# Kernel tuning notes

Hardware: AMD Instinct MI355X
Metric: run time of the kernel (lower is better)

## Reference

```python
import jax, jax.numpy as jnp
import numpy as np

N, E = 50000, 800000
NODE_DIM, EDGE_DIM = 128, 32
EGO_H, PEER_H, EDGE_H = 64, 64, 32  # node_hidden=128 split; edge_hidden=32


def setup_inputs() -> dict:
    key = jax.random.key(0)
    ks = jax.random.split(key, 9)
    x = jax.random.normal(ks[0], (N, NODE_DIM), dtype=jnp.float32)
    edge_attrs = jax.random.normal(ks[1], (E, EDGE_DIM), dtype=jnp.float32)
    edge_index = jax.random.randint(ks[2], (2, E), 0, N, dtype=jnp.int32)
    # Linear params (torch convention: W [out, in]), num_layers=1 -> single emb Linear per MLPLayer
    def lin(k, out_d, in_d):
        kw, kb = jax.random.split(k)
        s = 1.0 / np.sqrt(in_d)
        return (jax.random.uniform(kw, (out_d, in_d), minval=-s, maxval=s, dtype=jnp.float32),
                jax.random.uniform(kb, (out_d,), minval=-s, maxval=s, dtype=jnp.float32))
    W_peer, b_peer = lin(ks[3], PEER_H + EDGE_H, NODE_DIM + EDGE_DIM)
    W_ego, b_ego = lin(ks[4], EGO_H, NODE_DIM)
    W_edge, b_edge = lin(ks[5], EDGE_H, EDGE_DIM)
    return {"x": x, "edge_attrs": edge_attrs,
            "W_peer": W_peer, "b_peer": b_peer,
            "W_ego": W_ego, "b_ego": b_ego,
            "W_edge": W_edge, "b_edge": b_edge,
            "edge_index": edge_index}


def reference(x, edge_attrs, W_peer, b_peer, W_ego, b_ego, W_edge, b_edge, edge_index):
    n = x.shape[0]
    # adj_t = SparseTensor(row=ei[0], col=ei[1]).t() -> row = ei[1], col = ei[0]
    row = edge_index[1]
    col = edge_index[0]

    # ego branch
    h_ego = jax.nn.relu(x @ W_ego.T + b_ego)  # [N, EGO_H]

    # degree-based row normalization: deg^-0.5 per adj_t row, inf -> 0
    deg = jax.ops.segment_sum(jnp.ones((row.shape[0],), x.dtype), row, num_segments=n)
    dinv = jnp.where(deg > 0, jax.lax.rsqrt(jnp.maximum(deg, 1.0)) * (deg > 0), 0.0)
    dinv = jnp.where(deg > 0, deg ** -0.5, 0.0)
    norm_val = dinv[row]  # [E]

    # peer branch: gather x[row], cat edge_attrs, linear, normalize, scatter-sum over row
    peer_features = jnp.concatenate([x[row], edge_attrs], axis=1)  # [E, NODE_DIM+EDGE_DIM]
    peer_msg = norm_val[:, None] * (peer_features @ W_peer.T + b_peer)
    h_peer = jax.nn.relu(jax.ops.segment_sum(peer_msg, row, num_segments=n))  # [N, PEER_H+EDGE_H]

    # edge branch
    h_e = jax.nn.relu(edge_attrs @ W_edge.T + b_edge)  # [E, EDGE_H]
    h_e_agg = jax.ops.segment_sum(h_e, row, num_segments=n)  # adj_t.set_value(h_edge).sum(1)
    # norm.matmul(h_edge): out[i] = sum_{e: row[e]==i} norm_val[e] * h_e_agg[col[e]]
    h_e_mm = jax.ops.segment_sum(norm_val[:, None] * h_e_agg[col], row, num_segments=n)
    h_edge = jnp.concatenate([h_e_agg, h_e_mm], axis=1)  # [N, 2*EDGE_H]

    out = jnp.concatenate([h_ego, h_edge, h_peer], axis=1)  # [N, 224]
    return out
```

## Files before the change

kernel.cpp:

```cpp
#include <hip/hip_runtime.h>


typedef float f32x4 __attribute__((ext_vector_type(4)));
typedef short bf16x8 __attribute__((ext_vector_type(8)));
typedef unsigned short u16x8 __attribute__((ext_vector_type(8)));

#define BP 256

__device__ __forceinline__ unsigned short f2bf(float f) {
    unsigned u = __float_as_uint(f);
    u += 0x7fffu + ((u >> 16) & 1u);
    return (unsigned short)(u >> 16);
}
__device__ __forceinline__ float bf2f(unsigned short u) {
    return __uint_as_float((unsigned)u << 16);
}
__device__ __forceinline__ u16x8 pk8u(float4 lo, float4 hi) {
    u16x8 r;
    r[0]=f2bf(lo.x); r[1]=f2bf(lo.y); r[2]=f2bf(lo.z); r[3]=f2bf(lo.w);
    r[4]=f2bf(hi.x); r[5]=f2bf(hi.y); r[6]=f2bf(hi.z); r[7]=f2bf(hi.w);
    return r;
}
__device__ __forceinline__ bf16x8 mk_frag(ushort4 lo, ushort4 hi) {
    bf16x8 b;
    b[0]=(short)lo.x; b[1]=(short)lo.y; b[2]=(short)lo.z; b[3]=(short)lo.w;
    b[4]=(short)hi.x; b[5]=(short)hi.y; b[6]=(short)hi.z; b[7]=(short)hi.w;
    return b;
}
__device__ __forceinline__ bf16x8 ld_bfrag(const unsigned short* bp) {
    return mk_frag(*reinterpret_cast<const ushort4*>(bp),
                   *reinterpret_cast<const ushort4*>(bp + 16));
}

__global__ __launch_bounds__(256) void k_prepw(const float* __restrict__ W_ego,
                                               const float* __restrict__ W_peer,
                                               const float* __restrict__ W_edge,
                                               unsigned short* __restrict__ Bt,
                                               unsigned short* __restrict__ Bte,
                                               int* __restrict__ deg, int N) {
    int idx = blockIdx.x * blockDim.x + threadIdx.x;
    if (idx < 160 * 160) {
        int n = idx / 160, k = idx % 160;
        float v;
        if (n < 64) v = (k < 128) ? W_ego[n * 128 + k] : 0.f;
        else        v = W_peer[(n - 64) * 160 + k];
        Bt[idx] = f2bf(v);
    } else if (idx < 160 * 160 + 32 * 32) {
        int j = idx - 160 * 160;
        Bte[j] = f2bf(W_edge[j]);
    }
    if (idx < N) deg[idx] = 0;
}

__global__ __launch_bounds__(256) void k_hist(const int* __restrict__ row,
                                              int* __restrict__ deg,
                                              int* __restrict__ rank, int E) {
    int e = blockIdx.x * blockDim.x + threadIdx.x;
    if (e < E) rank[e] = atomicAdd(&deg[row[e]], 1);
}

__global__ __launch_bounds__(256) void k_scan_partial(const int* __restrict__ deg,
                                                      int* __restrict__ bsum, int N) {
    __shared__ int sh[256];
    int base = blockIdx.x * 1024 + threadIdx.x * 4;
    int s = 0;
#pragma unroll
    for (int q = 0; q < 4; ++q) { int i = base + q; if (i < N) s += deg[i]; }
    sh[threadIdx.x] = s;
    __syncthreads();
    for (int off = 128; off > 0; off >>= 1) {
        if (threadIdx.x < off) sh[threadIdx.x] += sh[threadIdx.x + off];
        __syncthreads();
    }
    if (threadIdx.x == 0) bsum[blockIdx.x] = sh[0];
}

__global__ __launch_bounds__(256) void k_scan_final(
    const int* __restrict__ deg, const int* __restrict__ bsum,
    int* __restrict__ off,
    float* __restrict__ sd, float* __restrict__ rdeg, int* __restrict__ nstart,
    float* __restrict__ eagg, float* __restrict__ sea, int N)
{
    __shared__ int sh[256];
    __shared__ int s_boff;
    int t = threadIdx.x;
    int NB = gridDim.x;

    if (t < 64) {
        int v = (t < NB) ? bsum[t] : 0;
        int p = (t < (int)blockIdx.x) ? v : 0;
#pragma unroll
        for (int m = 1; m < 64; m <<= 1) {
            p += __shfl_xor(p, m);
            v += __shfl_xor(v, m);
        }
        if (t == 0) {
            s_boff = p;
            if (blockIdx.x == 0) off[N] = v;
        }
    }
    __syncthreads();

    int base = blockIdx.x * 1024 + t * 4;
    int v[4];
#pragma unroll
    for (int q = 0; q < 4; ++q) v[q] = (base + q < N) ? deg[base + q] : 0;
    int ts = v[0] + v[1] + v[2] + v[3];
    sh[t] = ts;
    __syncthreads();
    int incl = ts;
    for (int d = 1; d < 256; d <<= 1) {
        int val = (t >= d) ? sh[t - d] : 0;
        __syncthreads();
        incl += val;
        sh[t] = incl;
        __syncthreads();
    }
    int running = s_boff + incl - ts;
#pragma unroll
    for (int q = 0; q < 4; ++q) {
        int i = base + q;
        if (i < N) {
            int s = running, e = running + v[q];
            off[i] = s;
            int dg = v[q];
            sd[i]   = dg > 0 ? sqrtf((float)dg) : 0.f;
            rdeg[i] = dg > 0 ? 1.f / (float)dg : 0.f;
            for (int b = (s + BP - 1) / BP; b * BP < e; ++b) nstart[b] = i;
            bool zneed = (dg == 0) || ((s / BP) != ((e - 1) / BP));
            if (zneed) {
                float4 z = {0.f, 0.f, 0.f, 0.f};
                float4* pe = reinterpret_cast<float4*>(eagg + (size_t)i * 32);
                float4* ps = reinterpret_cast<float4*>(sea  + (size_t)i * 32);
#pragma unroll
                for (int q2 = 0; q2 < 8; ++q2) { pe[q2] = z; ps[q2] = z; }
            }
            running = e;
        }
    }
}

__global__ __launch_bounds__(256) void k_scatcvt(
    const float* __restrict__ ea, const int* __restrict__ row,
    const int* __restrict__ col, const int* __restrict__ off,
    const int* __restrict__ rank,
    unsigned short* __restrict__ easorted,
    unsigned short* __restrict__ colsort, int E)
{
    int e = blockIdx.x * blockDim.x + threadIdx.x;
    if (e >= E) return;
    int pos = off[row[e]] + rank[e];
    const float4* src = reinterpret_cast<const float4*>(ea + (size_t)e * 32);
    u16x8* dst = reinterpret_cast<u16x8*>(easorted + (size_t)pos * 32);
#pragma unroll
    for (int q = 0; q < 4; ++q)
        dst[q] = pk8u(src[2 * q], src[2 * q + 1]);
    colsort[pos] = (unsigned short)col[e];
}

__global__ __launch_bounds__(512) void k_agg(
    const unsigned short* __restrict__ easorted,
    const int* __restrict__ off, const int* __restrict__ nstart,
    const unsigned short* __restrict__ Bte, const float* __restrict__ b_edge,
    float* __restrict__ eagg, float* __restrict__ sea, int N, int E)
{
    __shared__ unsigned short hs [BP][36];
    __shared__ unsigned short asr[BP][36];
    const int tid  = threadIdx.x;
    const int w    = tid >> 6;
    const int lane = tid & 63;
    const int n16  = lane & 15;
    const int h    = lane >> 4;
    const int P    = blockIdx.x * BP;

    {
        const int tA = w * 32 + n16;
        const int p0 = min(P + tA,      E - 1);
        const int p1 = min(P + tA + 16, E - 1);
        const unsigned short* r0 = easorted + (size_t)p0 * 32 + h * 4;
        const unsigned short* r1 = easorted + (size_t)p1 * 32 + h * 4;
        ushort4 lo0 = *reinterpret_cast<const ushort4*>(r0);
        ushort4 hi0 = *reinterpret_cast<const ushort4*>(r0 + 16);
        ushort4 lo1 = *reinterpret_cast<const ushort4*>(r1);
        ushort4 hi1 = *reinterpret_cast<const ushort4*>(r1 + 16);

        *reinterpret_cast<ushort4*>(&asr[tA][h * 4])           = lo0;
        *reinterpret_cast<ushort4*>(&asr[tA][16 + h * 4])      = hi0;
        *reinterpret_cast<ushort4*>(&asr[tA + 16][h * 4])      = lo1;
        *reinterpret_cast<ushort4*>(&asr[tA + 16][16 + h * 4]) = hi1;

        bf16x8 a0 = mk_frag(lo0, hi0);
        bf16x8 a1 = mk_frag(lo1, hi1);
        bf16x8 b0 = ld_bfrag(Bte + (size_t)n16 * 32 + h * 4);
        bf16x8 b1 = ld_bfrag(Bte + (size_t)(16 + n16) * 32 + h * 4);
        f32x4 d00 = {0.f,0.f,0.f,0.f}, d01 = {0.f,0.f,0.f,0.f};
        f32x4 d10 = {0.f,0.f,0.f,0.f}, d11 = {0.f,0.f,0.f,0.f};
        d00 = __builtin_amdgcn_mfma_f32_16x16x32_bf16(a0, b0, d00, 0, 0, 0);
        d01 = __builtin_amdgcn_mfma_f32_16x16x32_bf16(a0, b1, d01, 0, 0, 0);
        d10 = __builtin_amdgcn_mfma_f32_16x16x32_bf16(a1, b0, d10, 0, 0, 0);
        d11 = __builtin_amdgcn_mfma_f32_16x16x32_bf16(a1, b1, d11, 0, 0, 0);

        const int tr0 = w * 32 + h * 4;
        float be0 = b_edge[n16], be1 = b_edge[16 + n16];
#pragma unroll
        for (int r = 0; r < 4; ++r) {
            hs[tr0 + r][n16]           = f2bf(fmaxf(d00[r] + be0, 0.f));
            hs[tr0 + r][16 + n16]      = f2bf(fmaxf(d01[r] + be1, 0.f));
            hs[tr0 + 16 + r][n16]      = f2bf(fmaxf(d10[r] + be0, 0.f));
            hs[tr0 + 16 + r][16 + n16] = f2bf(fmaxf(d11[r] + be1, 0.f));
        }
    }
    __syncthreads();

    const int c = lane & 7, sub = lane >> 3;
    const int node0 = nstart[blockIdx.x];

    for (int n = node0 + w; n < N; n += 8) {
        int s0 = off[n];
        if (s0 >= P + BP) break;
        int e0 = off[n + 1];
        int s = max(s0, P) - P, eEnd = min(e0, P + BP) - P;
        float4 hv = {0.f,0.f,0.f,0.f}, av = {0.f,0.f,0.f,0.f};
        for (int t = s + sub; t < eEnd; t += 8) {
            ushort4 uh = *reinterpret_cast<const ushort4*>(&hs [t][c * 4]);
            ushort4 ua = *reinterpret_cast<const ushort4*>(&asr[t][c * 4]);
            hv.x += bf2f(uh.x); hv.y += bf2f(uh.y); hv.z += bf2f(uh.z); hv.w += bf2f(uh.w);
            av.x += bf2f(ua.x); av.y += bf2f(ua.y); av.z += bf2f(ua.z); av.w += bf2f(ua.w);
        }
#pragma unroll
        for (int m = 8; m < 64; m <<= 1) {
            hv.x += __shfl_xor(hv.x, m); hv.y += __shfl_xor(hv.y, m);
            hv.z += __shfl_xor(hv.z, m); hv.w += __shfl_xor(hv.w, m);
            av.x += __shfl_xor(av.x, m); av.y += __shfl_xor(av.y, m);
            av.z += __shfl_xor(av.z, m); av.w += __shfl_xor(av.w, m);
        }
        if (lane < 8) {
            float* pe = eagg + (size_t)n * 32 + c * 4;
            float* ps = sea  + (size_t)n * 32 + c * 4;
            bool interior = (s0 >= P) && (e0 <= P + BP);
            if (interior) {
                *reinterpret_cast<float4*>(pe) = hv;
                *reinterpret_cast<float4*>(ps) = av;
            } else {
                atomicAdd(pe+0,hv.x); atomicAdd(pe+1,hv.y);
                atomicAdd(pe+2,hv.z); atomicAdd(pe+3,hv.w);
                atomicAdd(ps+0,av.x); atomicAdd(ps+1,av.y);
                atomicAdd(ps+2,av.z); atomicAdd(ps+3,av.w);
            }
        }
    }
}

__global__ __launch_bounds__(256) void k_nodecvt(
    const float* __restrict__ x, const float* __restrict__ sea,
    const float* __restrict__ sd, const float* __restrict__ rdeg,
    const unsigned short* __restrict__ Bt,
    const float* __restrict__ b_ego, const float* __restrict__ b_peer,
    const float* __restrict__ eagg, unsigned short* __restrict__ eagg_bf,
    float* __restrict__ out, int N, int node_grid)
{
    if ((int)blockIdx.x >= node_grid) {
        int idx = (blockIdx.x - node_grid) * 256 + threadIdx.x;
        if (idx >= N * 8) return;
        int node = idx >> 3, c = idx & 7;
        float4 v = reinterpret_cast<const float4*>(eagg + (size_t)node * 32)[c];
        ushort4 u = {f2bf(v.x), f2bf(v.y), f2bf(v.z), f2bf(v.w)};
        *reinterpret_cast<ushort4*>(eagg_bf + (size_t)node * 32 + c * 4) = u;
        reinterpret_cast<float4*>(out + (size_t)node * 224 + 64)[c] = v;
        return;
    }
    const int lane = threadIdx.x & 63;
    const int wv   = threadIdx.x >> 6;
    const int wm   = blockIdx.x * 64 + wv * 16;
    const int n16  = lane & 15;
    const int h    = lane >> 4;

    const int m_l = min(wm + n16, N - 1);

    f32x4 acc[10];
#pragma unroll
    for (int f = 0; f < 10; ++f) acc[f] = (f32x4){0.f,0.f,0.f,0.f};

#pragma unroll
    for (int kc = 0; kc < 5; ++kc) {
        bf16x8 bfr[10];
#pragma unroll
        for (int f = 0; f < 10; ++f)
            bfr[f] = ld_bfrag(Bt + (size_t)(f * 16 + n16) * 160 + kc * 32 + h * 4);
        float4 lo, hi;
        if (kc < 4) {
            const float* ap = x + (size_t)m_l * 128 + kc * 32 + h * 4;
            lo = *reinterpret_cast<const float4*>(ap);
            hi = *reinterpret_cast<const float4*>(ap + 16);
        } else {
            float r = rdeg[m_l];
            const float* ap = sea + (size_t)m_l * 32 + h * 4;
            lo = *reinterpret_cast<const float4*>(ap);
            hi = *reinterpret_cast<const float4*>(ap + 16);
            lo.x*=r; lo.y*=r; lo.z*=r; lo.w*=r;
            hi.x*=r; hi.y*=r; hi.z*=r; hi.w*=r;
        }
        u16x8 au = pk8u(lo, hi);
        bf16x8 a;
#pragma unroll
        for (int q = 0; q < 8; ++q) a[q] = (short)au[q];
#pragma unroll
        for (int f = 0; f < 10; ++f)
            acc[f] = __builtin_amdgcn_mfma_f32_16x16x32_bf16(a, bfr[f], acc[f], 0, 0, 0);
    }

    const int r4 = h * 4;
    float sdv[4];
#pragma unroll
    for (int r = 0; r < 4; ++r) {
        int node = wm + r4 + r;
        sdv[r] = (node < N) ? sd[node] : 0.f;
    }
#pragma unroll
    for (int f = 0; f < 10; ++f) {
        int c = f * 16 + n16;
        float be = (c < 64)  ? b_ego[c] : 0.f;
        float bp = (c >= 64) ? b_peer[c - 64] : 0.f;
#pragma unroll
        for (int r = 0; r < 4; ++r) {
            int node = wm + r4 + r;
            if (node >= N) continue;
            float v = acc[f][r];
            if (c < 64)
                out[(size_t)node * 224 + c] = fmaxf(v + be, 0.f);
            else
                out[(size_t)node * 224 + 64 + c] = fmaxf(sdv[r] * (v + bp), 0.f);
        }
    }
}

__global__ __launch_bounds__(256) void k_mmagg(
    const unsigned short* __restrict__ colsort, const int* __restrict__ off,
    const unsigned short* __restrict__ eagg_bf, float* __restrict__ out, int N)
{
    int wid  = (blockIdx.x * blockDim.x + threadIdx.x) >> 6;
    int lane = threadIdx.x & 63;
    if (wid >= N) return;
    int s = off[wid], e = off[wid + 1];
    int c   = lane & 7;
    int sub = lane >> 3;
    float4 acc = {0.f, 0.f, 0.f, 0.f};
    float4 acc2 = {0.f, 0.f, 0.f, 0.f};
    for (int t0 = s; t0 < e; t0 += 16) {
        int t1 = t0 + sub, t2 = t0 + 8 + sub;
        if (t1 < e) {
            ushort4 u = *reinterpret_cast<const ushort4*>(
                eagg_bf + (size_t)colsort[t1] * 32 + c * 4);
            acc.x += bf2f(u.x); acc.y += bf2f(u.y);
            acc.z += bf2f(u.z); acc.w += bf2f(u.w);
        }
        if (t2 < e) {
            ushort4 u = *reinterpret_cast<const ushort4*>(
                eagg_bf + (size_t)colsort[t2] * 32 + c * 4);
            acc2.x += bf2f(u.x); acc2.y += bf2f(u.y);
            acc2.z += bf2f(u.z); acc2.w += bf2f(u.w);
        }
    }
    acc.x += acc2.x; acc.y += acc2.y; acc.z += acc2.z; acc.w += acc2.w;
#pragma unroll
    for (int m = 8; m < 64; m <<= 1) {
        acc.x += __shfl_xor(acc.x, m);
        acc.y += __shfl_xor(acc.y, m);
        acc.z += __shfl_xor(acc.z, m);
        acc.w += __shfl_xor(acc.w, m);
    }
    int dg = e - s;
    float dinv = dg > 0 ? rsqrtf((float)dg) : 0.f;
    if (lane < 8) {
        float4 o4 = {acc.x * dinv, acc.y * dinv, acc.z * dinv, acc.w * dinv};
        reinterpret_cast<float4*>(out + (size_t)wid * 224 + 96)[c] = o4;
    }
}

extern "C" void kernel_launch(void* const* d_in, const int* in_sizes, int n_in,
                              void* d_out, int out_size, void* d_ws, size_t ws_size,
                              hipStream_t stream)
{
    const float* x      = (const float*)d_in[0];
    const float* ea     = (const float*)d_in[1];
    const float* W_peer = (const float*)d_in[2];
    const float* b_peer = (const float*)d_in[3];
    const float* W_ego  = (const float*)d_in[4];
    const float* b_ego  = (const float*)d_in[5];
    const float* W_edge = (const float*)d_in[6];
    const float* b_edge = (const float*)d_in[7];
    const int*   ei     = (const int*)d_in[8];

    const int N = in_sizes[0] / 128;
    const int E = in_sizes[8] / 2;
    const int* col = ei;
    const int* row = ei + E;
    const int nblocks = (E + BP - 1) / BP;

    char* wp = (char*)d_ws;
    auto carve = [&](size_t bytes) { char* r = wp; wp += (bytes + 15) & ~(size_t)15; return r; };
    int*            rank     = (int*)carve((size_t)E * 4);
    unsigned short* easorted = (unsigned short*)carve((size_t)E * 64);
    unsigned short* colsort  = (unsigned short*)carve((size_t)E * 2);
    int*            deg_i    = (int*)carve((size_t)N * 4);
    float*          eagg     = (float*)carve((size_t)N * 128);
    float*          sea      = (float*)carve((size_t)N * 128);
    unsigned short* eagg_bf  = (unsigned short*)carve((size_t)N * 64);
    int*            off      = (int*)carve((size_t)(N + 1) * 4);
    int*            bsum     = (int*)carve(64 * 4);
    float*          sd       = (float*)carve((size_t)N * 4);
    float*          rdeg     = (float*)carve((size_t)N * 4);
    int*            nstart   = (int*)carve((size_t)nblocks * 4);
    unsigned short* Bt       = (unsigned short*)carve(160 * 160 * 2);
    unsigned short* Bte      = (unsigned short*)carve(32 * 32 * 2);
    float*          out      = (float*)d_out;

    const int TB = 256;
    const int NB = (N + 1023) / 1024;
    const int prepn = max(N, 160 * 160 + 32 * 32);
    k_prepw       <<<(prepn + TB - 1) / TB, TB, 0, stream>>>(W_ego, W_peer, W_edge,
                                                             Bt, Bte, deg_i, N);
    k_hist        <<<(E + TB - 1) / TB, TB, 0, stream>>>(row, deg_i, rank, E);
    k_scan_partial<<<NB, TB, 0, stream>>>(deg_i, bsum, N);
    k_scan_final  <<<NB, TB, 0, stream>>>(deg_i, bsum, off, sd, rdeg,
                                          nstart, eagg, sea, N);
    k_scatcvt     <<<(E + TB - 1) / TB, TB, 0, stream>>>(ea, row, col, off, rank,
                                                         easorted, colsort, E);

    k_agg<<<nblocks, 512, 0, stream>>>(easorted, off, nstart, Bte, b_edge,
                                       eagg, sea, N, E);

    const int node_grid = (N + 63) / 64;
    const int cvt_grid  = (N * 8 + TB - 1) / TB;
    k_nodecvt<<<node_grid + cvt_grid, TB, 0, stream>>>(x, sea, sd, rdeg, Bt,
                                                       b_ego, b_peer, eagg,
                                                       eagg_bf, out, N, node_grid);

    const int agg_grid = (N + 3) / 4;
    k_mmagg<<<agg_grid, TB, 0, stream>>>(colsort, off, eagg_bf, out, N);
}
```

Before: 190.5 us.

## Fuse edge-aggregate output and bf16 conversion into k_agg; vectorize scatter

k_agg now writes interior-node edge aggregates directly to the output and to the bf16 copy. The later conversion pass only handles nodes that span block boundaries or have zero degree, which it detects from offsets. k_scatcvt processes four edges per thread with vectorized int4 loads of row, rank and col. This is meant to cut redundant global reads and writes of the edge aggregate and reduce the launch and thread overhead of the scatter.

```diff
diff --git a/kernel.cpp b/kernel.cpp
--- a/kernel.cpp
+++ b/kernel.cpp
@@ -147,22 +147,46 @@
     unsigned short* __restrict__ easorted,
     unsigned short* __restrict__ colsort, int E)
 {
-    int e = blockIdx.x * blockDim.x + threadIdx.x;
-    if (e >= E) return;
-    int pos = off[row[e]] + rank[e];
-    const float4* src = reinterpret_cast<const float4*>(ea + (size_t)e * 32);
-    u16x8* dst = reinterpret_cast<u16x8*>(easorted + (size_t)pos * 32);
-#pragma unroll
-    for (int q = 0; q < 4; ++q)
-        dst[q] = pk8u(src[2 * q], src[2 * q + 1]);
-    colsort[pos] = (unsigned short)col[e];
+    int base = (blockIdx.x * 256 + threadIdx.x) * 4;
+    if (base >= E) return;
+    if (base + 3 < E) {
+        int4 r4 = *reinterpret_cast<const int4*>(row + base);
+        int4 k4 = *reinterpret_cast<const int4*>(rank + base);
+        int4 c4 = *reinterpret_cast<const int4*>(col + base);
+        int pos0 = off[r4.x] + k4.x;
+        int pos1 = off[r4.y] + k4.y;
+        int pos2 = off[r4.z] + k4.z;
+        int pos3 = off[r4.w] + k4.w;
+        int posv[4] = {pos0, pos1, pos2, pos3};
+        int colv[4] = {c4.x, c4.y, c4.z, c4.w};
+#pragma unroll
+        for (int j = 0; j < 4; ++j) {
+            const float4* src = reinterpret_cast<const float4*>(ea + (size_t)(base + j) * 32);
+            u16x8* dst = reinterpret_cast<u16x8*>(easorted + (size_t)posv[j] * 32);
+#pragma unroll
+            for (int q = 0; q < 4; ++q)
+                dst[q] = pk8u(src[2 * q], src[2 * q + 1]);
+            colsort[posv[j]] = (unsigned short)colv[j];
+        }
+    } else {
+        for (int e = base; e < E; ++e) {
+            int pos = off[row[e]] + rank[e];
+            const float4* src = reinterpret_cast<const float4*>(ea + (size_t)e * 32);
+            u16x8* dst = reinterpret_cast<u16x8*>(easorted + (size_t)pos * 32);
+#pragma unroll
+            for (int q = 0; q < 4; ++q)
+                dst[q] = pk8u(src[2 * q], src[2 * q + 1]);
+            colsort[pos] = (unsigned short)col[e];
+        }
+    }
 }
 
 __global__ __launch_bounds__(512) void k_agg(
     const unsigned short* __restrict__ easorted,
     const int* __restrict__ off, const int* __restrict__ nstart,
     const unsigned short* __restrict__ Bte, const float* __restrict__ b_edge,
-    float* __restrict__ eagg, float* __restrict__ sea, int N, int E)
+    float* __restrict__ eagg, float* __restrict__ sea,
+    unsigned short* __restrict__ eagg_bf, float* __restrict__ out, int N, int E)
 {
     __shared__ unsigned short hs [BP][36];
     __shared__ unsigned short asr[BP][36];
@@ -235,13 +259,15 @@
             av.z += __shfl_xor(av.z, m); av.w += __shfl_xor(av.w, m);
         }
         if (lane < 8) {
-            float* pe = eagg + (size_t)n * 32 + c * 4;
-            float* ps = sea  + (size_t)n * 32 + c * 4;
             bool interior = (s0 >= P) && (e0 <= P + BP);
+            float* ps = sea + (size_t)n * 32 + c * 4;
             if (interior) {
-                *reinterpret_cast<float4*>(pe) = hv;
+                *reinterpret_cast<float4*>(out + (size_t)n * 224 + 64 + c * 4) = hv;
+                ushort4 ub = {f2bf(hv.x), f2bf(hv.y), f2bf(hv.z), f2bf(hv.w)};
+                *reinterpret_cast<ushort4*>(eagg_bf + (size_t)n * 32 + c * 4) = ub;
                 *reinterpret_cast<float4*>(ps) = av;
             } else {
+                float* pe = eagg + (size_t)n * 32 + c * 4;
                 atomicAdd(pe+0,hv.x); atomicAdd(pe+1,hv.y);
                 atomicAdd(pe+2,hv.z); atomicAdd(pe+3,hv.w);
                 atomicAdd(ps+0,av.x); atomicAdd(ps+1,av.y);
@@ -257,12 +283,17 @@
     const unsigned short* __restrict__ Bt,
     const float* __restrict__ b_ego, const float* __restrict__ b_peer,
     const float* __restrict__ eagg, unsigned short* __restrict__ eagg_bf,
+    const int* __restrict__ off,
     float* __restrict__ out, int N, int node_grid)
 {
     if ((int)blockIdx.x >= node_grid) {
         int idx = (blockIdx.x - node_grid) * 256 + threadIdx.x;
         if (idx >= N * 8) return;
         int node = idx >> 3, c = idx & 7;
+        int s = off[node], e = off[node + 1];
+        int dg = e - s;
+        bool zneed = (dg == 0) || ((s / BP) != ((e - 1) / BP));
+        if (!zneed) return;
         float4 v = reinterpret_cast<const float4*>(eagg + (size_t)node * 32)[c];
         ushort4 u = {f2bf(v.x), f2bf(v.y), f2bf(v.z), f2bf(v.w)};
         *reinterpret_cast<ushort4*>(eagg_bf + (size_t)node * 32 + c * 4) = u;
@@ -424,17 +455,17 @@
     k_scan_partial<<<NB, TB, 0, stream>>>(deg_i, bsum, N);
     k_scan_final  <<<NB, TB, 0, stream>>>(deg_i, bsum, off, sd, rdeg,
                                           nstart, eagg, sea, N);
-    k_scatcvt     <<<(E + TB - 1) / TB, TB, 0, stream>>>(ea, row, col, off, rank,
-                                                         easorted, colsort, E);
+    k_scatcvt     <<<(E + TB * 4 - 1) / (TB * 4), TB, 0, stream>>>(ea, row, col, off, rank,
+                                                                   easorted, colsort, E);
 
     k_agg<<<nblocks, 512, 0, stream>>>(easorted, off, nstart, Bte, b_edge,
-                                       eagg, sea, N, E);
+                                       eagg, sea, eagg_bf, out, N, E);
 
     const int node_grid = (N + 63) / 64;
-    const int cvt_grid  = (N * 8 + TB - 1) / TB;
-    k_nodecvt<<<node_grid + cvt_grid, TB, 0, stream>>>(x, sea, sd, rdeg, Bt,
+    const int fin_grid  = (N * 8 + TB - 1) / TB;
+    k_nodecvt<<<node_grid + fin_grid, TB, 0, stream>>>(x, sea, sd, rdeg, Bt,
                                                        b_ego, b_peer, eagg,
-                                                       eagg_bf, out, N, node_grid);
+                                                       eagg_bf, off, out, N, node_grid);
 
     const int agg_grid = (N + 3) / 4;
     k_mmagg<<<agg_grid, TB, 0, stream>>>(colsort, off, eagg_bf, out, N);
```

New measurement: 197.8 us. +3.8%, slower.
